# Optimization experiments

Hardware: AMD Instinct MI355X
Metric: run time of the kernel (lower is better)

## Reference

```python
import jax, jax.numpy as jnp
import numpy as np

N_NODES = 20000
N_EDGES = 640000
D_IN = 128
D_HID = 128


def setup_inputs() -> dict:
    key = jax.random.key(0)
    ks = jax.random.split(key, 10)
    s_in = 1.0 / np.sqrt(D_IN).astype(np.float32)
    s_hid = 1.0 / np.sqrt(D_HID).astype(np.float32)
    return {
        "h": jax.random.normal(ks[0], (N_NODES, D_IN), jnp.float32),
        "edge_index": jax.random.randint(ks[1], (2, N_EDGES), 0, N_NODES, jnp.int32),
        "W0": jax.random.normal(ks[2], (D_IN, D_HID), jnp.float32) * s_in,
        "b0": jnp.zeros((D_HID,), jnp.float32),
        "W1": jax.random.normal(ks[3], (D_HID, D_HID), jnp.float32) * s_hid,
        "b1": jnp.zeros((D_HID,), jnp.float32),
        "W2": jax.random.normal(ks[4], (D_HID, D_HID), jnp.float32) * s_hid,
        "b2": jnp.zeros((D_HID,), jnp.float32),
        "W3": jax.random.normal(ks[5], (D_HID, D_HID), jnp.float32) * s_hid,
        "b3": jnp.zeros((D_HID,), jnp.float32),
    }


def reference(h, edge_index, W0, b0, W1, b1, W2, b2, W3, b3):
    # GIN forward: num_layers-1 = 4 GINConv layers, each
    # h' = Linear((1+eps)*h + sum_{j->i} h_j) with eps = 0.
    src = edge_index[0]
    dst = edge_index[1]
    n = h.shape[0]
    for W, b in ((W0, b0), (W1, b1), (W2, b2), (W3, b3)):
        # sparse sum-aggregation over edges: gather source features, scatter-add to dst
        agg = jax.ops.segment_sum(h[src], dst, num_segments=n)  # [N, D]
        h = (h + agg) @ W + b  # dense per-node MLP (single Linear)
    return h
```

## Files before the change

### kernel.cpp

```cpp
#include <hip/hip_runtime.h>

#define N_NODES 20000
#define N_EDGES 640000
#define D 128
#define CAP 128
#define NB_AGG 40000
#define NB_CHAIN 129
#define SPMV_BLOCKS 313
#define NB_H2BF 1250
#define NB_ZERO 79
#define TM 32

typedef unsigned int uint;

__device__ __forceinline__ float bflo(uint u) { return __uint_as_float(u << 16); }
__device__ __forceinline__ float bfhi(uint u) { return __uint_as_float(u & 0xffff0000u); }
__device__ __forceinline__ uint pack2bf(float lo, float hi) {
    uint a = __float_as_uint(lo), b = __float_as_uint(hi);
    a += 0x7fffu + ((a >> 16) & 1u);
    b += 0x7fffu + ((b >> 16) & 1u);
    return (a >> 16) | (b & 0xffff0000u);
}


__global__ void init_kernel(const float4* __restrict__ hin, uint4* __restrict__ hbf,
                            int* __restrict__ cnt) {
    int bid = blockIdx.x;
    int t = threadIdx.x;
    if (bid < NB_H2BF) {
        int i = bid * 256 + t;
        float4 f0 = hin[i * 2];
        float4 f1 = hin[i * 2 + 1];
        uint4 o;
        o.x = pack2bf(f0.x, f0.y); o.y = pack2bf(f0.z, f0.w);
        o.z = pack2bf(f1.x, f1.y); o.w = pack2bf(f1.z, f1.w);
        hbf[i] = o;
    } else {
        int i = (bid - NB_H2BF) * 256 + t;
        if (i < N_NODES) cnt[i] = 0;
    }
}


__global__ void scatter_direct_kernel(const int4* __restrict__ src4, const int4* __restrict__ dst4,
                                      int* __restrict__ cnt, int* __restrict__ slot) {
    int e4 = blockIdx.x * blockDim.x + threadIdx.x;
    if (e4 < N_EDGES / 4) {
        int4 s = src4[e4];
        int4 d = dst4[e4];
        slot[d.x * CAP + atomicAdd(&cnt[d.x], 1)] = s.x;
        slot[d.y * CAP + atomicAdd(&cnt[d.y], 1)] = s.y;
        slot[d.z * CAP + atomicAdd(&cnt[d.z], 1)] = s.z;
        slot[d.w * CAP + atomicAdd(&cnt[d.w], 1)] = s.w;
    }
}


__global__ __launch_bounds__(64) void agg_fused_kernel(
        const uint4* __restrict__ hbf, const int* __restrict__ cnt,
        const int* __restrict__ slot, uint4* __restrict__ xbf,
        const float* __restrict__ cA, const float* __restrict__ cbias,
        const float* __restrict__ cB, float* __restrict__ cO,
        const float* __restrict__ uin, float* __restrict__ uout) {
    int bid = blockIdx.x;
    int t = threadIdx.x;

    if (bid >= NB_AGG) {
        int cb = bid - NB_AGG;
        if (cO && cb < NB_CHAIN) {
            const float* Ar = (cb < 128) ? &cA[cb * 128] : cbias;
            int c0 = t, c1 = t + 64;
            float s0 = 0.f, s1 = 0.f;
            for (int k = 0; k < 128; ++k) {
                float a = Ar[k];
                s0 += a * cB[k * 128 + c0];
                s1 += a * cB[k * 128 + c1];
            }
            cO[cb * 128 + c0] = s0;
            cO[cb * 128 + c1] = s1;
        } else if (uout) {
            int sb = cb - (cO ? NB_CHAIN : 0);
            int node = sb * 64 + t;
            if (node < N_NODES) {
                int c = cnt[node];
                const int* sl = &slot[node * CAP];
                float s;
                if (uin) {
                    s = uin[node];
                    for (int k = 0; k < c; ++k) s += uin[sl[k]];
                } else {
                    s = 1.0f + 2.0f * (float)c;
                    for (int k = 0; k < c; ++k) s += (float)cnt[sl[k]];
                }
                uout[node] = s;
            }
        }
        return;
    }

    int r = bid & 7;
    int q = bid >> 3;
    int slice = r >> 2;
    int node  = q * 4 + (r & 3);
    int lo = node * CAP;
    int hi = lo + cnt[node];
    int slot8 = t >> 3;
    int fl    = t & 7;
    int soff  = slice * 8 + fl;

    uint4 sv = hbf[(size_t)node * 16 + soff];

    float a0 = 0.f, a1 = 0.f, a2 = 0.f, a3 = 0.f;
    float a4 = 0.f, a5 = 0.f, a6 = 0.f, a7 = 0.f;

#define ACC8(v) do { \
        a0 += bflo((v).x); a1 += bfhi((v).x); \
        a2 += bflo((v).y); a3 += bfhi((v).y); \
        a4 += bflo((v).z); a5 += bfhi((v).z); \
        a6 += bflo((v).w); a7 += bfhi((v).w); } while (0)

    int k = lo + slot8;
    for (; k + 24 < hi; k += 32) {
        int s0 = slot[k];
        int s1 = slot[k + 8];
        int s2 = slot[k + 16];
        int s3 = slot[k + 24];
        uint4 v0 = hbf[(size_t)s0 * 16 + soff];
        uint4 v1 = hbf[(size_t)s1 * 16 + soff];
        uint4 v2 = hbf[(size_t)s2 * 16 + soff];
        uint4 v3 = hbf[(size_t)s3 * 16 + soff];
        ACC8(v0); ACC8(v1); ACC8(v2); ACC8(v3);
    }
    for (; k < hi; k += 8) {
        int s0 = slot[k];
        uint4 v0 = hbf[(size_t)s0 * 16 + soff];
        ACC8(v0);
    }
#undef ACC8

    a0 += __shfl_xor(a0, 8);  a1 += __shfl_xor(a1, 8);
    a2 += __shfl_xor(a2, 8);  a3 += __shfl_xor(a3, 8);
    a4 += __shfl_xor(a4, 8);  a5 += __shfl_xor(a5, 8);
    a6 += __shfl_xor(a6, 8);  a7 += __shfl_xor(a7, 8);
    a0 += __shfl_xor(a0, 16); a1 += __shfl_xor(a1, 16);
    a2 += __shfl_xor(a2, 16); a3 += __shfl_xor(a3, 16);
    a4 += __shfl_xor(a4, 16); a5 += __shfl_xor(a5, 16);
    a6 += __shfl_xor(a6, 16); a7 += __shfl_xor(a7, 16);
    a0 += __shfl_xor(a0, 32); a1 += __shfl_xor(a1, 32);
    a2 += __shfl_xor(a2, 32); a3 += __shfl_xor(a3, 32);
    a4 += __shfl_xor(a4, 32); a5 += __shfl_xor(a5, 32);
    a6 += __shfl_xor(a6, 32); a7 += __shfl_xor(a7, 32);

    if (t < 8) {
        a0 += bflo(sv.x); a1 += bfhi(sv.x);
        a2 += bflo(sv.y); a3 += bfhi(sv.y);
        a4 += bflo(sv.z); a5 += bfhi(sv.z);
        a6 += bflo(sv.w); a7 += bfhi(sv.w);
        uint4 o;
        o.x = pack2bf(a0, a1); o.y = pack2bf(a2, a3);
        o.z = pack2bf(a4, a5); o.w = pack2bf(a6, a7);
        xbf[(size_t)node * 16 + soff] = o;
    }
}


__global__ __launch_bounds__(256) void gemm_kernel(const uint4* __restrict__ xb,
                                                   const float* __restrict__ W,
                                                   float* __restrict__ out,
                                                   const int* __restrict__ cnt,
                                                   const float* __restrict__ ub,
                                                   const float* __restrict__ uc,
                                                   const float* __restrict__ v2p,
                                                   const float* __restrict__ v3p,
                                                   const float* __restrict__ v4p,
                                                   const float* __restrict__ v1p) {
    __shared__ float Xs[TM][D];
    int t = threadIdx.x;
    int row0 = blockIdx.x * TM;

    for (int i = t; i < TM * 16; i += 256) {
        int rr  = i >> 4;
        int c16 = i & 15;
        uint4 u = xb[(size_t)(row0 + rr) * 16 + c16];
        float4 f0 = make_float4(bflo(u.x), bfhi(u.x), bflo(u.y), bfhi(u.y));
        float4 f1 = make_float4(bflo(u.z), bfhi(u.z), bflo(u.w), bfhi(u.w));
        *((float4*)&Xs[rr][c16 * 8])     = f0;
        *((float4*)&Xs[rr][c16 * 8 + 4]) = f1;
    }
    __syncthreads();

    int cg = t & 31;
    int rg = t >> 5;
    int j0 = cg * 4;
    int r0 = rg * 4;

    float acc[4][4];
    #pragma unroll
    for (int i = 0; i < 4; ++i) {
        acc[i][0] = 0.f; acc[i][1] = 0.f; acc[i][2] = 0.f; acc[i][3] = 0.f;
    }

    for (int k4 = 0; k4 < D; k4 += 4) {
        float4 w0 = *((const float4*)&W[(k4 + 0) * D + j0]);
        float4 w1 = *((const float4*)&W[(k4 + 1) * D + j0]);
        float4 w2 = *((const float4*)&W[(k4 + 2) * D + j0]);
        float4 w3 = *((const float4*)&W[(k4 + 3) * D + j0]);
        #pragma unroll
        for (int i = 0; i < 4; ++i) {
            float4 xv = *((const float4*)&Xs[r0 + i][k4]);
            acc[i][0] += xv.x * w0.x; acc[i][0] += xv.y * w1.x;
            acc[i][0] += xv.z * w2.x; acc[i][0] += xv.w * w3.x;
            acc[i][1] += xv.x * w0.y; acc[i][1] += xv.y * w1.y;
            acc[i][1] += xv.z * w2.y; acc[i][1] += xv.w * w3.y;
            acc[i][2] += xv.x * w0.z; acc[i][2] += xv.y * w1.z;
            acc[i][2] += xv.z * w2.z; acc[i][2] += xv.w * w3.z;
            acc[i][3] += xv.x * w0.w; acc[i][3] += xv.y * w1.w;
            acc[i][3] += xv.z * w2.w; acc[i][3] += xv.w * w3.w;
        }
    }

    float4 v1 = *((const float4*)&v1p[j0]);
    float4 v2 = *((const float4*)&v2p[j0]);
    float4 v3 = *((const float4*)&v3p[j0]);
    float4 v4 = *((const float4*)&v4p[j0]);

    #pragma unroll
    for (int i = 0; i < 4; ++i) {
        int ra = row0 + r0 + i;
        float aa = 1.0f + (float)cnt[ra];
        float ab = ub[ra], ac = uc[ra];
        float o0 = acc[i][0] + ac * v4.x + ab * v3.x + aa * v2.x + v1.x;
        float o1 = acc[i][1] + ac * v4.y + ab * v3.y + aa * v2.y + v1.y;
        float o2 = acc[i][2] + ac * v4.z + ab * v3.z + aa * v2.z + v1.z;
        float o3 = acc[i][3] + ac * v4.w + ab * v3.w + aa * v2.w + v1.w;
        *((float4*)&out[(size_t)ra * D + j0]) = make_float4(o0, o1, o2, o3);
    }
}


extern "C" void kernel_launch(void* const* d_in, const int* in_sizes, int n_in,
                              void* d_out, int out_size, void* d_ws, size_t ws_size,
                              hipStream_t stream) {
    const float* h   = (const float*)d_in[0];
    const int*   ei  = (const int*)d_in[1];
    const int*   src = ei;
    const int*   dst = ei + N_EDGES;
    const float* W0 = (const float*)d_in[2]; const float* b0 = (const float*)d_in[3];
    const float* W1 = (const float*)d_in[4]; const float* b1 = (const float*)d_in[5];
    const float* W2 = (const float*)d_in[6]; const float* b2 = (const float*)d_in[7];
    const float* W3 = (const float*)d_in[8]; const float* b3 = (const float*)d_in[9];
    float* out = (float*)d_out;

    char* ws = (char*)d_ws;
    auto alloc = [&](size_t bytes) {
        char* p = ws;
        ws += (bytes + 255) & ~(size_t)255;
        return p;
    };
    int*   cnt     = (int*)alloc(N_NODES * sizeof(int));
    int*   slot    = (int*)alloc((size_t)N_NODES * CAP * sizeof(int));
    uint4* hbf     = (uint4*)alloc((size_t)N_NODES * 16 * sizeof(uint4));
    uint4* bufA    = (uint4*)alloc((size_t)N_NODES * 16 * sizeof(uint4));
    uint4* bufB    = (uint4*)alloc((size_t)N_NODES * 16 * sizeof(uint4));
    float* T2      = (float*)alloc(129 * D * sizeof(float));
    float* T3      = (float*)alloc(129 * D * sizeof(float));
    float* TW      = (float*)alloc(129 * D * sizeof(float));
    float* ub      = (float*)alloc(N_NODES * sizeof(float));
    float* uc      = (float*)alloc(N_NODES * sizeof(float));

    init_kernel<<<NB_H2BF + NB_ZERO, 256, 0, stream>>>((const float4*)h, hbf, cnt);

    scatter_direct_kernel<<<(N_EDGES / 4 + 255) / 256, 256, 0, stream>>>(
        (const int4*)src, (const int4*)dst, cnt, slot);

    agg_fused_kernel<<<NB_AGG + NB_CHAIN + SPMV_BLOCKS, 64, 0, stream>>>(
        hbf, cnt, slot, bufA, W2, b2, W3, T2, nullptr, ub);
    agg_fused_kernel<<<NB_AGG + NB_CHAIN + SPMV_BLOCKS, 64, 0, stream>>>(
        bufA, cnt, slot, bufB, W1, b1, T2, T3, ub, uc);
    agg_fused_kernel<<<NB_AGG + NB_CHAIN, 64, 0, stream>>>(
        bufB, cnt, slot, bufA, W0, b0, T3, TW, nullptr, nullptr);
    agg_fused_kernel<<<NB_AGG, 64, 0, stream>>>(
        bufA, cnt, slot, bufB, nullptr, nullptr, nullptr, nullptr, nullptr, nullptr);

    gemm_kernel<<<N_NODES / TM, 256, 0, stream>>>(
        bufB, TW, out, cnt, ub, uc,
        T2 + 128 * D, T3 + 128 * D, TW + 128 * D, b3);
}
```

Baseline: 239.2 us.

## Store neighbor slots as 16-bit indices and overlap scatter with bf16 conversion

The CSR-like slot table now holds unsigned short source indices instead of int, which halves its footprint and the bytes read by every aggregation pass. This relies on N_NODES (20000) fitting in 16 bits. The bf16 conversion of h moves out of the init kernel into the same launch as the edge scatter, and a small separate kernel zeroes the counters. Scatter and conversion blocks therefore run concurrently, at the cost of one extra tiny launch.

```diff
diff --git a/kernel.cpp b/kernel.cpp
--- a/kernel.cpp
+++ b/kernel.cpp
@@ -7,11 +7,12 @@
 #define NB_AGG 40000
 #define NB_CHAIN 129
 #define SPMV_BLOCKS 313
+#define NB_SCAT 625
 #define NB_H2BF 1250
-#define NB_ZERO 79
 #define TM 32
 
 typedef unsigned int uint;
+typedef unsigned short ushort;
 
 __device__ __forceinline__ float bflo(uint u) { return __uint_as_float(u << 16); }
 __device__ __forceinline__ float bfhi(uint u) { return __uint_as_float(u & 0xffff0000u); }
@@ -23,42 +24,40 @@
 }
 
 
-__global__ void init_kernel(const float4* __restrict__ hin, uint4* __restrict__ hbf,
-                            int* __restrict__ cnt) {
+__global__ void zero_cnt_kernel(int* __restrict__ cnt) {
+    int i = blockIdx.x * blockDim.x + threadIdx.x;
+    if (i < N_NODES) cnt[i] = 0;
+}
+
+
+__global__ void scatter_h2bf_kernel(const int4* __restrict__ src4, const int4* __restrict__ dst4,
+                                    int* __restrict__ cnt, ushort* __restrict__ slot,
+                                    const float4* __restrict__ hin, uint4* __restrict__ hbf) {
     int bid = blockIdx.x;
     int t = threadIdx.x;
-    if (bid < NB_H2BF) {
-        int i = bid * 256 + t;
+    if (bid < NB_SCAT) {
+        int e4 = bid * 256 + t;
+        int4 s = src4[e4];
+        int4 d = dst4[e4];
+        slot[d.x * CAP + atomicAdd(&cnt[d.x], 1)] = (ushort)s.x;
+        slot[d.y * CAP + atomicAdd(&cnt[d.y], 1)] = (ushort)s.y;
+        slot[d.z * CAP + atomicAdd(&cnt[d.z], 1)] = (ushort)s.z;
+        slot[d.w * CAP + atomicAdd(&cnt[d.w], 1)] = (ushort)s.w;
+    } else {
+        int i = (bid - NB_SCAT) * 256 + t;
         float4 f0 = hin[i * 2];
         float4 f1 = hin[i * 2 + 1];
         uint4 o;
         o.x = pack2bf(f0.x, f0.y); o.y = pack2bf(f0.z, f0.w);
         o.z = pack2bf(f1.x, f1.y); o.w = pack2bf(f1.z, f1.w);
         hbf[i] = o;
-    } else {
-        int i = (bid - NB_H2BF) * 256 + t;
-        if (i < N_NODES) cnt[i] = 0;
-    }
-}
-
-
-__global__ void scatter_direct_kernel(const int4* __restrict__ src4, const int4* __restrict__ dst4,
-                                      int* __restrict__ cnt, int* __restrict__ slot) {
-    int e4 = blockIdx.x * blockDim.x + threadIdx.x;
-    if (e4 < N_EDGES / 4) {
-        int4 s = src4[e4];
-        int4 d = dst4[e4];
-        slot[d.x * CAP + atomicAdd(&cnt[d.x], 1)] = s.x;
-        slot[d.y * CAP + atomicAdd(&cnt[d.y], 1)] = s.y;
-        slot[d.z * CAP + atomicAdd(&cnt[d.z], 1)] = s.z;
-        slot[d.w * CAP + atomicAdd(&cnt[d.w], 1)] = s.w;
     }
 }
 
 
 __global__ __launch_bounds__(64) void agg_fused_kernel(
         const uint4* __restrict__ hbf, const int* __restrict__ cnt,
-        const int* __restrict__ slot, uint4* __restrict__ xbf,
+        const ushort* __restrict__ slot, uint4* __restrict__ xbf,
         const float* __restrict__ cA, const float* __restrict__ cbias,
         const float* __restrict__ cB, float* __restrict__ cO,
         const float* __restrict__ uin, float* __restrict__ uout) {
@@ -83,7 +82,7 @@
             int node = sb * 64 + t;
             if (node < N_NODES) {
                 int c = cnt[node];
-                const int* sl = &slot[node * CAP];
+                const ushort* sl = &slot[node * CAP];
                 float s;
                 if (uin) {
                     s = uin[node];
@@ -257,21 +256,21 @@
         ws += (bytes + 255) & ~(size_t)255;
         return p;
     };
-    int*   cnt     = (int*)alloc(N_NODES * sizeof(int));
-    int*   slot    = (int*)alloc((size_t)N_NODES * CAP * sizeof(int));
-    uint4* hbf     = (uint4*)alloc((size_t)N_NODES * 16 * sizeof(uint4));
-    uint4* bufA    = (uint4*)alloc((size_t)N_NODES * 16 * sizeof(uint4));
-    uint4* bufB    = (uint4*)alloc((size_t)N_NODES * 16 * sizeof(uint4));
-    float* T2      = (float*)alloc(129 * D * sizeof(float));
-    float* T3      = (float*)alloc(129 * D * sizeof(float));
-    float* TW      = (float*)alloc(129 * D * sizeof(float));
-    float* ub      = (float*)alloc(N_NODES * sizeof(float));
-    float* uc      = (float*)alloc(N_NODES * sizeof(float));
-
-    init_kernel<<<NB_H2BF + NB_ZERO, 256, 0, stream>>>((const float4*)h, hbf, cnt);
-
-    scatter_direct_kernel<<<(N_EDGES / 4 + 255) / 256, 256, 0, stream>>>(
-        (const int4*)src, (const int4*)dst, cnt, slot);
+    int*    cnt  = (int*)alloc(N_NODES * sizeof(int));
+    ushort* slot = (ushort*)alloc((size_t)N_NODES * CAP * sizeof(ushort));
+    uint4*  hbf  = (uint4*)alloc((size_t)N_NODES * 16 * sizeof(uint4));
+    uint4*  bufA = (uint4*)alloc((size_t)N_NODES * 16 * sizeof(uint4));
+    uint4*  bufB = (uint4*)alloc((size_t)N_NODES * 16 * sizeof(uint4));
+    float*  T2   = (float*)alloc(129 * D * sizeof(float));
+    float*  T3   = (float*)alloc(129 * D * sizeof(float));
+    float*  TW   = (float*)alloc(129 * D * sizeof(float));
+    float*  ub   = (float*)alloc(N_NODES * sizeof(float));
+    float*  uc   = (float*)alloc(N_NODES * sizeof(float));
+
+    zero_cnt_kernel<<<(N_NODES + 255) / 256, 256, 0, stream>>>(cnt);
+
+    scatter_h2bf_kernel<<<NB_SCAT + NB_H2BF, 256, 0, stream>>>(
+        (const int4*)src, (const int4*)dst, cnt, slot, (const float4*)h, hbf);
 
     agg_fused_kernel<<<NB_AGG + NB_CHAIN + SPMV_BLOCKS, 64, 0, stream>>>(
         hbf, cnt, slot, bufA, W2, b2, W3, T2, nullptr, ub);
```

After: 236.0 us. No clear change (-1.3%).
